# Optimization experiments

Hardware: AMD Instinct MI355X
Metric: run time of the kernel (lower is better)

## Reference

```python
import jax, jax.numpy as jnp
import numpy as np

B, S, D, H, E = 4, 2048, 1024, 4096, 8
TOP_K = 2


def setup_inputs() -> dict:
    key = jax.random.key(0)
    k = jax.random.split(key, 7)
    scale_in = 1.0 / np.sqrt(D)
    scale_h = 1.0 / np.sqrt(H)
    return {
        "x": jax.random.normal(k[0], (B, S, D), jnp.float32),
        "Wr": jax.random.normal(k[1], (D, E), jnp.float32) * scale_in,
        "br": jnp.zeros((E,), jnp.float32),
        "W1": jax.random.normal(k[2], (E, D, H), jnp.float32) * scale_in,
        "b1": jnp.zeros((E, H), jnp.float32),
        "W2": jax.random.normal(k[3], (E, H, D), jnp.float32) * scale_h,
        "b2": jnp.zeros((E, D), jnp.float32),
    }


def reference(x, Wr, br, W1, b1, W2, b2):
    # Router: softmax over experts, then top-k and renormalize.
    routing = jax.nn.softmax(x @ Wr + br, axis=-1)            # [B,S,E]
    topk_vals, topk_idx = jax.lax.top_k(routing, TOP_K)        # [B,S,K]
    topk_norm = topk_vals / jnp.sum(topk_vals, axis=-1, keepdims=True)
    # Scatter normalized top-k weights back to a dense [B,S,E] gate.
    gate = jnp.sum(jax.nn.one_hot(topk_idx, E, dtype=x.dtype) * topk_norm[..., None], axis=2)  # [B,S,E]
    # Per-expert FFN over all tokens (original's dense masked loop; masked-out
    # tokens have gate==0 so zeroing inputs is mathematically equivalent).
    h = jax.nn.relu(jnp.einsum("bsd,edh->ebsh", x, W1) + b1[:, None, None, :])  # [E,B,S,H]
    y = jnp.einsum("ebsh,ehd->ebsd", h, W2) + b2[:, None, None, :]              # [E,B,S,D]
    out = jnp.einsum("ebsd,bse->bsd", y, gate)                                   # [B,S,D]
    return out
```

## Files before the change

kernel.cpp:

```cpp
#include <hip/hip_runtime.h>
#include <stdint.h>

typedef unsigned short u16;
typedef __attribute__((ext_vector_type(8))) short s8bf;
typedef __attribute__((ext_vector_type(4))) float f32x4;

#define N_TOK 8192
#define DIM   1024
#define HID   4096
#define NE    8
#define MAX_SLOTS 17408
#define MAX_TILES 160
#define TSTR  264

#define OFF_W1T  ((size_t)0)
#define OFF_Y    ((size_t)0)
#define OFF_W2T  ((size_t)67108864)
#define OFF_XB   ((size_t)134217728)
#define OFF_H    ((size_t)150994944)
#define OFF_TOS  ((size_t)293601280)
#define OFF_SOT  ((size_t)293670912)
#define OFF_TKI  ((size_t)293740544)
#define OFF_TKW  ((size_t)293806080)
#define OFF_CNT  ((size_t)293871616)
#define OFF_POF  ((size_t)293871680)
#define OFF_CUR  ((size_t)293871744)
#define OFF_NT   ((size_t)293871808)
#define OFF_TE   ((size_t)293871872)
#define OFF_TS   ((size_t)293872896)

__device__ __forceinline__ u16 f2b(float v) {
  union { float f; uint32_t u; } c; c.f = v;
  uint32_t u = c.u;
  return (u16)((u + 0x7FFFu + ((u >> 16) & 1u)) >> 16);
}
__device__ __forceinline__ float b2f(u16 b) {
  union { uint32_t u; float f; } c; c.u = ((uint32_t)b) << 16; return c.f;
}

typedef const __attribute__((address_space(1))) uint32_t* gp32;
typedef __attribute__((address_space(3))) uint32_t* lp32;
__device__ __forceinline__ void gl_lds16(const u16* g, u16* l) {
  __builtin_amdgcn_global_load_lds((gp32)(const void*)g, (lp32)(void*)l, 16, 0, 0);
}

__global__ __launch_bounds__(256) void transpose_to_bf16(
    const float* __restrict__ in, u16* __restrict__ out, int R, int C) {
  __shared__ u16 L[64 * TSTR];
  int tiles_c = C >> 6, tiles_r = R >> 8;
  int per = tiles_c * tiles_r;
  int e = blockIdx.x / per, t = blockIdx.x % per;
  int tr = t / tiles_c, tc = t % tiles_c;
  const float* ip = in + (size_t)e * R * C + (size_t)(tr * 256) * C + tc * 64;
  u16* op = out + (size_t)e * R * C + (size_t)(tc * 64) * R + tr * 256;
  const int tid = threadIdx.x;
  const int c = tid & 63;
  const int rb0 = (tid >> 6) * 8;
  #pragma unroll
  for (int p = 0; p < 8; p++) {
    int rb = p * 32 + rb0;
    u16 tmp[8];
    #pragma unroll
    for (int j = 0; j < 8; j++) tmp[j] = f2b(ip[(size_t)(rb + j) * C + c]);
    *(uint4*)&L[c * TSTR + rb] = *(const uint4*)tmp;
  }
  __syncthreads();
  const int s = tid & 31, ocb = tid >> 5;
  #pragma unroll
  for (int p = 0; p < 8; p++) {
    int oc = p * 8 + ocb;
    uint4 v = *(const uint4*)&L[oc * TSTR + s * 8];
    *(uint4*)&op[(size_t)oc * R + s * 8] = v;
  }
}

__global__ __launch_bounds__(256) void convert_x(const float* __restrict__ x,
                                                 u16* __restrict__ xb) {
  size_t i = ((size_t)blockIdx.x * 256 + threadIdx.x) * 8;
  float4 v0 = *(const float4*)(x + i);
  float4 v1 = *(const float4*)(x + i + 4);
  u16 o[8] = {f2b(v0.x), f2b(v0.y), f2b(v0.z), f2b(v0.w),
              f2b(v1.x), f2b(v1.y), f2b(v1.z), f2b(v1.w)};
  *(uint4*)(xb + i) = *(const uint4*)o;
}

__global__ __launch_bounds__(256) void router_kernel(
    const float* __restrict__ x, const float* __restrict__ Wr,
    const float* __restrict__ br, int* __restrict__ tki, float* __restrict__ tkw,
    int* __restrict__ counts) {
  int wave = threadIdx.x >> 6, lane = threadIdx.x & 63;
  int t = blockIdx.x * 4 + wave;
  const float* xr = x + (size_t)t * DIM;
  float acc[8] = {0.f, 0.f, 0.f, 0.f, 0.f, 0.f, 0.f, 0.f};
  #pragma unroll
  for (int i = 0; i < 16; i++) {
    int d = lane + i * 64;
    float xv = xr[d];
    float4 wa = *(const float4*)(Wr + d * 8);
    float4 wb = *(const float4*)(Wr + d * 8 + 4);
    acc[0] += xv * wa.x; acc[1] += xv * wa.y; acc[2] += xv * wa.z; acc[3] += xv * wa.w;
    acc[4] += xv * wb.x; acc[5] += xv * wb.y; acc[6] += xv * wb.z; acc[7] += xv * wb.w;
  }
  #pragma unroll
  for (int e = 0; e < 8; e++)
    #pragma unroll
    for (int off = 32; off >= 1; off >>= 1)
      acc[e] += __shfl_xor(acc[e], off, 64);
  if (lane == 0) {
    float l[8];
    #pragma unroll
    for (int e = 0; e < 8; e++) l[e] = acc[e] + br[e];
    float l0 = -1e30f; int i0 = 0;
    #pragma unroll
    for (int e = 0; e < 8; e++) if (l[e] > l0) { l0 = l[e]; i0 = e; }
    float l1 = -1e30f; int i1 = 0;
    #pragma unroll
    for (int e = 0; e < 8; e++) if (e != i0 && l[e] > l1) { l1 = l[e]; i1 = e; }
    float w0 = 1.f / (1.f + expf(l1 - l0));
    tki[t * 2] = i0; tki[t * 2 + 1] = i1;
    tkw[t * 2] = w0; tkw[t * 2 + 1] = 1.f - w0;
    atomicAdd(&counts[i0], 1);
    atomicAdd(&counts[i1], 1);
  }
}

__global__ void plan_kernel(const int* __restrict__ counts, int* __restrict__ poff,
                            int* __restrict__ cursor, int* __restrict__ ntiles,
                            int* __restrict__ tile_e, int* __restrict__ tile_s0) {
  int e = threadIdx.x;
  if (e < NE) {
    int po = 0, tb = 0;
    for (int i = 0; i < e; i++) {
      int tl = (counts[i] + 127) >> 7;
      po += tl << 7; tb += tl;
    }
    poff[e] = po;
    cursor[e] = 0;
    int tl = (counts[e] + 127) >> 7;
    for (int j = 0; j < tl; j++) { tile_e[tb + j] = e; tile_s0[tb + j] = po + j * 128; }
    if (e == NE - 1) ntiles[0] = tb + tl;
  }
}

__global__ __launch_bounds__(256) void scatter_kernel(
    const int* __restrict__ tki, const int* __restrict__ poff,
    int* __restrict__ cursor, int* __restrict__ token_of_slot,
    int* __restrict__ slot_of_token) {
  int t = blockIdx.x * 256 + threadIdx.x;
  #pragma unroll
  for (int k = 0; k < 2; k++) {
    int e = tki[t * 2 + k];
    int r = atomicAdd(&cursor[e], 1);
    int s = poff[e] + r;
    token_of_slot[s] = t;
    slot_of_token[t * 2 + k] = s;
  }
}

template <int MODE>
__global__ __launch_bounds__(512, 2) void moe_gemm(
    const u16* __restrict__ A, const u16* __restrict__ Bt,
    const float* __restrict__ bias, u16* __restrict__ Hout,
    const int* __restrict__ tile_e, const int* __restrict__ tile_s0,
    const int* __restrict__ ntiles, const int* __restrict__ token_of_slot,
    int K, int N, int NB) {
  __shared__ u16 SM[49152];

  const int nblk = blockIdx.x % NB;
  const int tileid = blockIdx.x / NB;
  if (tileid >= ntiles[0]) return;
  const int e = tile_e[tileid];
  const int slot0 = tile_s0[tileid];
  const int n0 = nblk * 256;
  const int T = K >> 6;

  const int tid = threadIdx.x;
  const int lane = tid & 63;
  const int wave = tid >> 6;
  const int wm = wave >> 2;
  const int wn = wave & 3;

  const int srow = tid >> 3;
  const int sslot = tid & 7;
  const u16* aB[2];
  #pragma unroll
  for (int l = 0; l < 2; l++) {
    int row = l * 64 + srow;
    int scol = (sslot ^ (row & 7)) * 8;
    int arow;
    if (MODE == 1) { int t0 = token_of_slot[slot0 + row]; arow = t0 < 0 ? 0 : t0; }
    else arow = slot0 + row;
    aB[l] = A + (size_t)arow * K + scol;
  }
  const u16* bE = Bt + (size_t)e * N * K;
  const u16* bB[4];
  #pragma unroll
  for (int l = 0; l < 4; l++) {
    int row = l * 64 + srow;
    int scol = (sslot ^ (row & 7)) * 8;
    bB[l] = bE + (size_t)(n0 + row) * K + scol;
  }

  const int colq = lane & 15;
  float bv[4];
  #pragma unroll
  for (int n = 0; n < 4; n++) bv[n] = bias[(size_t)e * N + n0 + wn * 64 + n * 16 + colq];
  asm volatile("s_waitcnt vmcnt(0)" ::: "memory");

  const int wb = wave * 64;
  #pragma unroll
  for (int tt = 0; tt < 2; tt++) {
    const int kq = tt * 64;
    u16* LA = SM + tt * 8192;
    u16* LB = SM + 16384 + tt * 16384;
    gl_lds16(aB[0] + kq, LA + wb * 8);
    gl_lds16(aB[1] + kq, LA + (512 + wb) * 8);
    gl_lds16(bB[0] + kq, LB + wb * 8);
    gl_lds16(bB[1] + kq, LB + (512 + wb) * 8);
    gl_lds16(bB[2] + kq, LB + (1024 + wb) * 8);
    gl_lds16(bB[3] + kq, LB + (1536 + wb) * 8);
  }
  asm volatile("s_waitcnt vmcnt(6)" ::: "memory");
  __builtin_amdgcn_s_barrier();

  const int q4 = lane >> 4;
  const int sx = lane & 7;
  const int sk0 = (q4 ^ sx) * 8;
  const int sk1 = sk0 ^ 32;
  const int aOff = (wm * 64 + (lane & 15)) * 64;
  const int bOff = (wn * 64 + (lane & 15)) * 64;

  f32x4 acc[4][4];
  #pragma unroll
  for (int i = 0; i < 4; i++)
    #pragma unroll
    for (int j = 0; j < 4; j++) acc[i][j] = (f32x4){0.f, 0.f, 0.f, 0.f};

  int kk = 128;
  for (int t = 0; t < T; ++t) {
    const int cb = t & 1;
    const u16* LA = SM + cb * 8192;
    const u16* LB = SM + 16384 + cb * 16384;
    u16* sLA = SM + cb * 8192;
    u16* sLB = SM + 16384 + cb * 16384;
    s8bf af[4][2], bf[4][2];

    #pragma unroll
    for (int m = 0; m < 4; m++) af[m][0] = *(const s8bf*)&LA[aOff + m * 1024 + sk0];
    #pragma unroll
    for (int n = 0; n < 4; n++) bf[n][0] = *(const s8bf*)&LB[bOff + n * 1024 + sk0];
    __builtin_amdgcn_s_barrier();
    __builtin_amdgcn_s_setprio(1);
    #pragma unroll
    for (int m = 0; m < 4; m++)
      #pragma unroll
      for (int n = 0; n < 2; n++)
        acc[m][n] = __builtin_amdgcn_mfma_f32_16x16x32_bf16(af[m][0], bf[n][0], acc[m][n], 0, 0, 0);
    __builtin_amdgcn_s_setprio(0);
    __builtin_amdgcn_s_barrier();

    #pragma unroll
    for (int m = 0; m < 4; m++) af[m][1] = *(const s8bf*)&LA[aOff + m * 1024 + sk1];
    #pragma unroll
    for (int n = 0; n < 4; n++) bf[n][1] = *(const s8bf*)&LB[bOff + n * 1024 + sk1];
    __builtin_amdgcn_s_barrier();
    __builtin_amdgcn_s_setprio(1);
    #pragma unroll
    for (int m = 0; m < 4; m++)
      #pragma unroll
      for (int n = 2; n < 4; n++)
        acc[m][n] = __builtin_amdgcn_mfma_f32_16x16x32_bf16(af[m][0], bf[n][0], acc[m][n], 0, 0, 0);
    __builtin_amdgcn_s_setprio(0);
    asm volatile("s_waitcnt lgkmcnt(0)" ::: "memory");
    __builtin_amdgcn_s_barrier();

    if (t + 2 < T) {
      gl_lds16(aB[0] + kk, sLA + wb * 8);
      gl_lds16(aB[1] + kk, sLA + (512 + wb) * 8);
      gl_lds16(bB[0] + kk, sLB + wb * 8);
    }
    __builtin_amdgcn_s_barrier();
    __builtin_amdgcn_s_setprio(1);
    #pragma unroll
    for (int m = 0; m < 4; m++)
      #pragma unroll
      for (int n = 0; n < 2; n++)
        acc[m][n] = __builtin_amdgcn_mfma_f32_16x16x32_bf16(af[m][1], bf[n][1], acc[m][n], 0, 0, 0);
    __builtin_amdgcn_s_setprio(0);
    __builtin_amdgcn_s_barrier();

    if (t + 2 < T) {
      gl_lds16(bB[1] + kk, sLB + (512 + wb) * 8);
      gl_lds16(bB[2] + kk, sLB + (1024 + wb) * 8);
      gl_lds16(bB[3] + kk, sLB + (1536 + wb) * 8);
    }
    __builtin_amdgcn_s_barrier();
    __builtin_amdgcn_s_setprio(1);
    #pragma unroll
    for (int m = 0; m < 4; m++)
      #pragma unroll
      for (int n = 2; n < 4; n++)
        acc[m][n] = __builtin_amdgcn_mfma_f32_16x16x32_bf16(af[m][1], bf[n][1], acc[m][n], 0, 0, 0);
    __builtin_amdgcn_s_setprio(0);
    if (t < T - 2)       asm volatile("s_waitcnt vmcnt(6)" ::: "memory");
    else if (t == T - 2) asm volatile("s_waitcnt vmcnt(0)" ::: "memory");
    __builtin_amdgcn_s_barrier();
    kk += 64;
  }

  #pragma unroll
  for (int m = 0; m < 4; m++) {
    __syncthreads();
    const int rbase = wm * 16 + ((lane >> 4) << 2);
    #pragma unroll
    for (int n = 0; n < 4; n++) {
      const int lcol = wn * 64 + n * 16 + colq;
      #pragma unroll
      for (int r = 0; r < 4; r++) {
        float v = acc[m][n][r] + bv[n];
        if (MODE == 1) v = fmaxf(v, 0.f);
        SM[(rbase + r) * 264 + lcol] = f2b(v);
      }
    }
    __syncthreads();
    #pragma unroll
    for (int it = 0; it < 2; it++) {
      const int idx = it * 512 + tid;
      const int rl = idx >> 5;
      const int c16 = (idx & 31) * 8;
      const int grow = (rl < 16) ? (m * 16 + rl) : (48 + m * 16 + rl);
      uint4 v = *(const uint4*)&SM[rl * 264 + c16];
      *(uint4*)&Hout[(size_t)(slot0 + grow) * N + n0 + c16] = v;
    }
  }
}

__global__ __launch_bounds__(256) void combine_kernel(
    const u16* __restrict__ y, const int* __restrict__ sot,
    const float* __restrict__ tkw, float* __restrict__ out) {
  int wave = threadIdx.x >> 6, lane = threadIdx.x & 63;
  int t = blockIdx.x * 4 + wave;
  int s0 = sot[t * 2], s1 = sot[t * 2 + 1];
  float w0 = tkw[t * 2], w1 = tkw[t * 2 + 1];
  const u16* y0 = y + (size_t)s0 * DIM;
  const u16* y1 = y + (size_t)s1 * DIM;
  float* op = out + (size_t)t * DIM;
  #pragma unroll
  for (int i = 0; i < 4; i++) {
    int d = i * 256 + lane * 4;
    uint2 a = *(const uint2*)(y0 + d);
    uint2 b = *(const uint2*)(y1 + d);
    float4 o;
    o.x = w0 * b2f((u16)(a.x & 0xFFFF)) + w1 * b2f((u16)(b.x & 0xFFFF));
    o.y = w0 * b2f((u16)(a.x >> 16))    + w1 * b2f((u16)(b.x >> 16));
    o.z = w0 * b2f((u16)(a.y & 0xFFFF)) + w1 * b2f((u16)(b.y & 0xFFFF));
    o.w = w0 * b2f((u16)(a.y >> 16))    + w1 * b2f((u16)(b.y >> 16));
    *(float4*)(op + d) = o;
  }
}

extern "C" void kernel_launch(void* const* d_in, const int* in_sizes, int n_in,
                              void* d_out, int out_size, void* d_ws, size_t ws_size,
                              hipStream_t stream) {
  const float* x  = (const float*)d_in[0];
  const float* Wr = (const float*)d_in[1];
  const float* br = (const float*)d_in[2];
  const float* W1 = (const float*)d_in[3];
  const float* b1 = (const float*)d_in[4];
  const float* W2 = (const float*)d_in[5];
  const float* b2 = (const float*)d_in[6];
  float* out = (float*)d_out;
  char* ws = (char*)d_ws;

  u16*   W1t  = (u16*)(ws + OFF_W1T);
  u16*   W2t  = (u16*)(ws + OFF_W2T);
  u16*   ybuf = (u16*)(ws + OFF_Y);
  u16*   xb   = (u16*)(ws + OFF_XB);
  u16*   hbuf = (u16*)(ws + OFF_H);
  int*   tos  = (int*)(ws + OFF_TOS);
  int*   sot  = (int*)(ws + OFF_SOT);
  int*   tki  = (int*)(ws + OFF_TKI);
  float* tkw  = (float*)(ws + OFF_TKW);
  int*   cnt  = (int*)(ws + OFF_CNT);
  int*   pof  = (int*)(ws + OFF_POF);
  int*   cur  = (int*)(ws + OFF_CUR);
  int*   nt   = (int*)(ws + OFF_NT);
  int*   te   = (int*)(ws + OFF_TE);
  int*   ts   = (int*)(ws + OFF_TS);

  hipMemsetAsync(tos, 0xFF, (size_t)MAX_SLOTS * sizeof(int), stream);
  hipMemsetAsync(cnt, 0, 8 * sizeof(int), stream);

  transpose_to_bf16<<<dim3(NE * (DIM / 256) * (HID / 64)), 256, 0, stream>>>(W1, W1t, DIM, HID);
  transpose_to_bf16<<<dim3(NE * (HID / 256) * (DIM / 64)), 256, 0, stream>>>(W2, W2t, HID, DIM);
  convert_x<<<dim3(N_TOK * DIM / (256 * 8)), 256, 0, stream>>>(x, xb);
  router_kernel<<<dim3(N_TOK / 4), 256, 0, stream>>>(x, Wr, br, tki, tkw, cnt);
  plan_kernel<<<dim3(1), 64, 0, stream>>>(cnt, pof, cur, nt, te, ts);
  scatter_kernel<<<dim3(N_TOK / 256), 256, 0, stream>>>(tki, pof, cur, tos, sot);

  moe_gemm<1><<<dim3((MAX_SLOTS / 128) * (HID / 256)), 512, 0, stream>>>(
      xb, W1t, b1, hbuf, te, ts, nt, tos, DIM, HID, HID / 256);
  moe_gemm<2><<<dim3((MAX_SLOTS / 128) * (DIM / 256)), 512, 0, stream>>>(
      hbuf, W2t, b2, ybuf, te, ts, nt, tos, HID, DIM, DIM / 256);
  combine_kernel<<<dim3(N_TOK / 4), 256, 0, stream>>>(ybuf, sot, tkw, out);
}
```

Before: 1.041 ms.

## Restructure GEMM main loop into two phases with fewer barriers

Reorganizes the K-loop of the grouped GEMM from four MFMA phases into two. Each phase reads both k-halves of its A/B fragments from LDS and then issues all its MFMAs. All six global-to-LDS prefetches are issued together after the compute, and the trailing barrier is skipped on the final iteration. sched_barrier calls pin instruction ordering around the s_barriers. The aim is to cut barrier count per iteration and give longer uninterrupted MFMA runs. In exchange, more fragment registers are live at once and memory-load/compute interleaving is coarser.

After: 1.048 ms. About the same (+0.7%).

```diff
diff --git a/kernel.cpp b/kernel.cpp
--- a/kernel.cpp
+++ b/kernel.cpp
@@ -246,65 +246,65 @@
     s8bf af[4][2], bf[4][2];
 
     #pragma unroll
-    for (int m = 0; m < 4; m++) af[m][0] = *(const s8bf*)&LA[aOff + m * 1024 + sk0];
-    #pragma unroll
-    for (int n = 0; n < 4; n++) bf[n][0] = *(const s8bf*)&LB[bOff + n * 1024 + sk0];
+    for (int m = 0; m < 4; m++) {
+      af[m][0] = *(const s8bf*)&LA[aOff + m * 1024 + sk0];
+      af[m][1] = *(const s8bf*)&LA[aOff + m * 1024 + sk1];
+    }
+    #pragma unroll
+    for (int n = 0; n < 2; n++) {
+      bf[n][0] = *(const s8bf*)&LB[bOff + n * 1024 + sk0];
+      bf[n][1] = *(const s8bf*)&LB[bOff + n * 1024 + sk1];
+    }
+    __builtin_amdgcn_sched_barrier(0);
     __builtin_amdgcn_s_barrier();
     __builtin_amdgcn_s_setprio(1);
     #pragma unroll
-    for (int m = 0; m < 4; m++)
+    for (int ks = 0; ks < 2; ks++)
       #pragma unroll
-      for (int n = 0; n < 2; n++)
-        acc[m][n] = __builtin_amdgcn_mfma_f32_16x16x32_bf16(af[m][0], bf[n][0], acc[m][n], 0, 0, 0);
+      for (int m = 0; m < 4; m++)
+        #pragma unroll
+        for (int n = 0; n < 2; n++)
+          acc[m][n] = __builtin_amdgcn_mfma_f32_16x16x32_bf16(af[m][ks], bf[n][ks],
+                                                              acc[m][n], 0, 0, 0);
     __builtin_amdgcn_s_setprio(0);
     __builtin_amdgcn_s_barrier();
 
     #pragma unroll
-    for (int m = 0; m < 4; m++) af[m][1] = *(const s8bf*)&LA[aOff + m * 1024 + sk1];
-    #pragma unroll
-    for (int n = 0; n < 4; n++) bf[n][1] = *(const s8bf*)&LB[bOff + n * 1024 + sk1];
+    for (int n = 2; n < 4; n++) {
+      bf[n][0] = *(const s8bf*)&LB[bOff + n * 1024 + sk0];
+      bf[n][1] = *(const s8bf*)&LB[bOff + n * 1024 + sk1];
+    }
+    __builtin_amdgcn_sched_barrier(0);
     __builtin_amdgcn_s_barrier();
     __builtin_amdgcn_s_setprio(1);
     #pragma unroll
-    for (int m = 0; m < 4; m++)
+    for (int ks = 0; ks < 2; ks++)
       #pragma unroll
-      for (int n = 2; n < 4; n++)
-        acc[m][n] = __builtin_amdgcn_mfma_f32_16x16x32_bf16(af[m][0], bf[n][0], acc[m][n], 0, 0, 0);
+      for (int m = 0; m < 4; m++)
+        #pragma unroll
+        for (int n = 2; n < 4; n++)
+          acc[m][n] = __builtin_amdgcn_mfma_f32_16x16x32_bf16(af[m][ks], bf[n][ks],
+                                                              acc[m][n], 0, 0, 0);
     __builtin_amdgcn_s_setprio(0);
     asm volatile("s_waitcnt lgkmcnt(0)" ::: "memory");
+    __builtin_amdgcn_sched_barrier(0);
     __builtin_amdgcn_s_barrier();
 
     if (t + 2 < T) {
       gl_lds16(aB[0] + kk, sLA + wb * 8);
       gl_lds16(aB[1] + kk, sLA + (512 + wb) * 8);
       gl_lds16(bB[0] + kk, sLB + wb * 8);
-    }
-    __builtin_amdgcn_s_barrier();
-    __builtin_amdgcn_s_setprio(1);
-    #pragma unroll
-    for (int m = 0; m < 4; m++)
-      #pragma unroll
-      for (int n = 0; n < 2; n++)
-        acc[m][n] = __builtin_amdgcn_mfma_f32_16x16x32_bf16(af[m][1], bf[n][1], acc[m][n], 0, 0, 0);
-    __builtin_amdgcn_s_setprio(0);
-    __builtin_amdgcn_s_barrier();
-
-    if (t + 2 < T) {
       gl_lds16(bB[1] + kk, sLB + (512 + wb) * 8);
       gl_lds16(bB[2] + kk, sLB + (1024 + wb) * 8);
       gl_lds16(bB[3] + kk, sLB + (1536 + wb) * 8);
     }
-    __builtin_amdgcn_s_barrier();
-    __builtin_amdgcn_s_setprio(1);
-    #pragma unroll
-    for (int m = 0; m < 4; m++)
-      #pragma unroll
-      for (int n = 2; n < 4; n++)
-        acc[m][n] = __builtin_amdgcn_mfma_f32_16x16x32_bf16(af[m][1], bf[n][1], acc[m][n], 0, 0, 0);
-    __builtin_amdgcn_s_setprio(0);
+    __builtin_amdgcn_sched_barrier(0);
     if (t < T - 2)       asm volatile("s_waitcnt vmcnt(6)" ::: "memory");
     else if (t == T - 2) asm volatile("s_waitcnt vmcnt(0)" ::: "memory");
-    __builtin_amdgcn_s_barrier();
+    if (t < T - 1) {
+      __builtin_amdgcn_sched_barrier(0);
+      __builtin_amdgcn_s_barrier();
+    }
     kk += 64;
   }
 
```
